# Kernel tuning notes

Hardware: AMD Instinct MI355X
Metric: run time of the kernel (lower is better)

The kernel has to match this reference:

```python
import jax, jax.numpy as jnp
import numpy as np

B, V = 256, 128000


def setup_inputs() -> dict:
    key = jax.random.key(0)
    k1, k2 = jax.random.split(key)
    logits = jax.random.normal(k1, (B, V), dtype=jnp.float32)
    temperatures = jax.random.uniform(k2, (B,), dtype=jnp.float32)
    return {"logits": logits, "temperatures": temperatures}


def reference(logits, temperatures):
    # logits: (B, V) float32, temperatures: (B,) float32
    logits = logits.astype(jnp.float32)
    # greedy path (temperature == 0)
    greedy_tokens = jnp.argmax(logits, axis=-1)
    # temperature-scaled softmax; guard t==0 (torch divides by 0 -> nan probs,
    # but the final where() discards that lane, so safe-div is math-equivalent)
    t = temperatures[:, None]
    safe_t = jnp.where(t == 0.0, 1.0, t)
    probs = jax.nn.softmax(logits / safe_t, axis=-1)  # (B, V)
    # Gumbel-max trick as in torch: argmax(probs / Exp(1) noise)
    noise = jax.random.exponential(jax.random.key(1), probs.shape, dtype=jnp.float32)
    sample_tokens = jnp.argmax(probs / noise, axis=-1)
    return jnp.where(temperatures == 0.0, greedy_tokens, sample_tokens)
```

## Files before the change

### kernel.cpp

```cpp
#include <hip/hip_runtime.h>
#include <stdint.h>
#include <math.h>

constexpr int BROWS = 256;
constexpr int VCOLS = 128000;
constexpr int NQ    = 5;
constexpr int QCOLS = VCOLS / NQ;
constexpr int QV4   = QCOLS / 4;
constexpr int NBLK  = BROWS * NQ;
constexpr int NTHR  = 320;
constexpr int NITER = QV4 / (NTHR * 4);

__device__ __forceinline__ uint32_t fmap(float v) {
  uint32_t b = __float_as_uint(v);
  return b ^ (uint32_t)(((int32_t)b >> 31) | 0x80000000);
}

__device__ __forceinline__ unsigned long long mkkey(uint32_t s, int idx) {
  return ((unsigned long long)s << 32) | (uint32_t)(~(uint32_t)idx);
}

__device__ __forceinline__ uint32_t rotl(uint32_t x, uint32_t r) {
  return __builtin_amdgcn_alignbit(x, x, 32u - r);
}

__device__ __forceinline__ void tf4_bits(uint32_t i0, uint32_t i1, uint32_t i2,
                                         uint32_t i3, uint32_t o[4]) {
  uint32_t a0, a1, a2, a3;
  uint32_t b0 = i0, b1 = i1, b2 = i2, b3 = i3;
#define RND(r) \
  a0 += b0; b0 = rotl(b0, r) ^ a0; \
  a1 += b1; b1 = rotl(b1, r) ^ a1; \
  a2 += b2; b2 = rotl(b2, r) ^ a2; \
  a3 += b3; b3 = rotl(b3, r) ^ a3;
  a0 = b0; b0 = rotl(b0, 13u) ^ a0;
  a1 = b1; b1 = rotl(b1, 13u) ^ a1;
  a2 = b2; b2 = rotl(b2, 13u) ^ a2;
  a3 = b3; b3 = rotl(b3, 13u) ^ a3;
  RND(15u) RND(26u) RND(6u)
  a0 += 1u; a1 += 1u; a2 += 1u; a3 += 1u;
  b0 += 0x1BD11BDCu; b1 += 0x1BD11BDCu; b2 += 0x1BD11BDCu; b3 += 0x1BD11BDCu;
  RND(17u) RND(29u) RND(16u) RND(24u)
  a0 += 0x1BD11BDBu; a1 += 0x1BD11BDBu; a2 += 0x1BD11BDBu; a3 += 0x1BD11BDBu;
  b0 += 2u; b1 += 2u; b2 += 2u; b3 += 2u;
  RND(13u) RND(15u) RND(26u) RND(6u)
  b0 += 4u; b1 += 4u; b2 += 4u; b3 += 4u;
  RND(17u) RND(29u) RND(16u) RND(24u)
  a0 += 1u; a1 += 1u; a2 += 1u; a3 += 1u;
  b0 += 0x1BD11BDFu; b1 += 0x1BD11BDFu; b2 += 0x1BD11BDFu; b3 += 0x1BD11BDFu;
  RND(13u) RND(15u) RND(26u) RND(6u)
  a0 += 0x1BD11BDBu; a1 += 0x1BD11BDBu; a2 += 0x1BD11BDBu; a3 += 0x1BD11BDBu;
  b0 += 5u; b1 += 5u; b2 += 5u; b3 += 5u;
#undef RND
  o[0] = a0 ^ b0; o[1] = a1 ^ b1; o[2] = a2 ^ b2; o[3] = a3 ^ b3;
}

template <int NT>
__device__ __forceinline__ unsigned long long blockMaxU64(unsigned long long v) {
  __shared__ unsigned long long s_w[NT / 64];
  const int wid = threadIdx.x >> 6, lane = threadIdx.x & 63;
  #pragma unroll
  for (int off = 32; off > 0; off >>= 1) {
    unsigned long long o = __shfl_xor(v, off, 64);
    if (o > v) v = o;
  }
  if (lane == 0) s_w[wid] = v;
  __syncthreads();
  if (threadIdx.x == 0) {
    #pragma unroll
    for (int w = 1; w < NT / 64; ++w) if (s_w[w] > v) v = s_w[w];
    s_w[0] = v;
  }
  __syncthreads();
  return s_w[0];
}

extern "C" __global__ void __launch_bounds__(NTHR)
k_main(const float* __restrict__ logits,
       const float* __restrict__ temps,
       unsigned long long* __restrict__ gPart,
       unsigned long long* __restrict__ sPart)
{
  const int blk = blockIdx.x;
  const int row = blk / NQ, q = blk % NQ;
  const float4* base =
      reinterpret_cast<const float4*>(logits + (size_t)row * VCOLS + q * QCOLS);

  const float t = temps[row];
  const float safe_t = (t == 0.0f) ? 1.0f : t;
  const float c1 = (1.0f / safe_t) * 1.4426950408889634f;

  const uint32_t rowbase = (uint32_t)row * (uint32_t)VCOLS;
  const uint32_t Ce = rowbase + (uint32_t)(q * QCOLS) + 1u;

  float gv = -INFINITY; uint32_t gx = 0u;
  float bv = -INFINITY; uint32_t bx = 0u;

  int vb = (int)threadIdx.x;
  float4 A0 = base[vb], A1 = base[vb + NTHR],
         A2 = base[vb + 2 * NTHR], A3 = base[vb + 3 * NTHR];

  #pragma unroll 1
  for (int it = 0; it < NITER; ++it) {
    const int nvb = vb + 4 * NTHR;
    float4 B0, B1, B2, B3;
    if (it + 1 < NITER) {
      B0 = base[nvb]; B1 = base[nvb + NTHR];
      B2 = base[nvb + 2 * NTHR]; B3 = base[nvb + 3 * NTHR];
    }

    const float4 As[4] = {A0, A1, A2, A3};
    #pragma unroll
    for (int u = 0; u < 4; ++u) {
      const uint32_t ce = Ce + (uint32_t)((vb + u * NTHR) * 4);
      const float lx[4] = {As[u].x, As[u].y, As[u].z, As[u].w};
      uint32_t bits[4];
      tf4_bits(ce, ce + 1u, ce + 2u, ce + 3u, bits);
      #pragma unroll
      for (uint32_t k = 0; k < 4; ++k) {
        const uint32_t x1i = ce + k;
        float f = __uint_as_float((bits[k] >> 9) | 0x3F800000u);
        float g = __builtin_amdgcn_logf(2.0f - f);
        float g2 = __builtin_amdgcn_logf(fabsf(g));
        float val = fmaf(lx[k], c1, -g2);
        if (lx[k] > gv) { gv = lx[k]; gx = x1i; }
        if (val  > bv) { bv = val;    bx = x1i; }
      }
    }

    vb = nvb;
    A0 = B0; A1 = B1; A2 = B2; A3 = B3;
  }

  const int gcol = (int)(gx - 1u - rowbase);
  const int scol = (int)(bx - 1u - rowbase);
  unsigned long long gk = blockMaxU64<NTHR>(mkkey(fmap(gv), gcol));
  unsigned long long sk = blockMaxU64<NTHR>(mkkey(fmap(bv), scol));
  if (threadIdx.x == 0) { gPart[blk] = gk; sPart[blk] = sk; }
}

extern "C" __global__ void __launch_bounds__(BROWS)
k3_final(const float* __restrict__ temps,
         const unsigned long long* __restrict__ gPart,
         const unsigned long long* __restrict__ sPart,
         int* __restrict__ out)
{
  const int r = threadIdx.x;
  if (r >= BROWS) return;
  unsigned long long g = gPart[r * NQ];
  unsigned long long s = sPart[r * NQ];
  #pragma unroll
  for (int j = 1; j < NQ; ++j) {
    unsigned long long og = gPart[r * NQ + j];
    unsigned long long os = sPart[r * NQ + j];
    if (og > g) g = og;
    if (os > s) s = os;
  }
  const int greedy = (int)(~(uint32_t)g);
  const int samp   = (int)(~(uint32_t)s);
  out[r] = (temps[r] == 0.0f) ? greedy : samp;
}

extern "C" void kernel_launch(void* const* d_in, const int* in_sizes, int n_in,
                              void* d_out, int out_size, void* d_ws, size_t ws_size,
                              hipStream_t stream) {
  const float* logits = (const float*)d_in[0];
  const float* temps  = (const float*)d_in[1];
  int* out = (int*)d_out;

  unsigned long long* gPart = (unsigned long long*)d_ws;
  unsigned long long* sPart = gPart + NBLK;

  k_main<<<NBLK, NTHR, 0, stream>>>(logits, temps, gPart, sPart);
  k3_final<<<1, BROWS, 0, stream>>>(temps, gPart, sPart, out);
}
```

Before: 81.72 us.

## Split greedy argmax into separate kernel run only for zero-temperature rows

Takes the greedy argmax tracking out of the main sampling loop. A new kernel computes the greedy max only for rows whose temperature is zero and returns early for all other rows. The row split doubles from 5 to 10 chunks, with a 2-deep float4 prefetch in place of 4-deep, to give more blocks. The cost is an extra kernel launch and a second read of the logits for any greedy rows. The random test temperatures are almost never exactly zero, so in practice that kernel mostly exits.

```diff
diff --git a/kernel.cpp b/kernel.cpp
--- a/kernel.cpp
+++ b/kernel.cpp
@@ -4,12 +4,12 @@
 
 constexpr int BROWS = 256;
 constexpr int VCOLS = 128000;
-constexpr int NQ    = 5;
+constexpr int NQ    = 10;
 constexpr int QCOLS = VCOLS / NQ;
 constexpr int QV4   = QCOLS / 4;
 constexpr int NBLK  = BROWS * NQ;
 constexpr int NTHR  = 320;
-constexpr int NITER = QV4 / (NTHR * 4);
+constexpr int NITER = QV4 / (NTHR * 2);
 
 __device__ __forceinline__ uint32_t fmap(float v) {
   uint32_t b = __float_as_uint(v);
@@ -78,7 +78,6 @@
 extern "C" __global__ void __launch_bounds__(NTHR)
 k_main(const float* __restrict__ logits,
        const float* __restrict__ temps,
-       unsigned long long* __restrict__ gPart,
        unsigned long long* __restrict__ sPart)
 {
   const int blk = blockIdx.x;
@@ -93,50 +92,73 @@
   const uint32_t rowbase = (uint32_t)row * (uint32_t)VCOLS;
   const uint32_t Ce = rowbase + (uint32_t)(q * QCOLS) + 1u;
 
-  float gv = -INFINITY; uint32_t gx = 0u;
   float bv = -INFINITY; uint32_t bx = 0u;
 
   int vb = (int)threadIdx.x;
-  float4 A0 = base[vb], A1 = base[vb + NTHR],
-         A2 = base[vb + 2 * NTHR], A3 = base[vb + 3 * NTHR];
+  float4 A0 = base[vb], A1 = base[vb + NTHR];
 
   #pragma unroll 1
   for (int it = 0; it < NITER; ++it) {
-    const int nvb = vb + 4 * NTHR;
-    float4 B0, B1, B2, B3;
+    const int nvb = vb + 2 * NTHR;
+    float4 B0, B1;
     if (it + 1 < NITER) {
       B0 = base[nvb]; B1 = base[nvb + NTHR];
-      B2 = base[nvb + 2 * NTHR]; B3 = base[nvb + 3 * NTHR];
     }
 
-    const float4 As[4] = {A0, A1, A2, A3};
+    const float4 As[2] = {A0, A1};
     #pragma unroll
-    for (int u = 0; u < 4; ++u) {
+    for (int u = 0; u < 2; ++u) {
       const uint32_t ce = Ce + (uint32_t)((vb + u * NTHR) * 4);
       const float lx[4] = {As[u].x, As[u].y, As[u].z, As[u].w};
       uint32_t bits[4];
       tf4_bits(ce, ce + 1u, ce + 2u, ce + 3u, bits);
       #pragma unroll
       for (uint32_t k = 0; k < 4; ++k) {
-        const uint32_t x1i = ce + k;
         float f = __uint_as_float((bits[k] >> 9) | 0x3F800000u);
         float g = __builtin_amdgcn_logf(2.0f - f);
         float g2 = __builtin_amdgcn_logf(fabsf(g));
         float val = fmaf(lx[k], c1, -g2);
-        if (lx[k] > gv) { gv = lx[k]; gx = x1i; }
-        if (val  > bv) { bv = val;    bx = x1i; }
+        if (val > bv) { bv = val; bx = ce + k; }
       }
     }
 
     vb = nvb;
-    A0 = B0; A1 = B1; A2 = B2; A3 = B3;
+    A0 = B0; A1 = B1;
   }
 
-  const int gcol = (int)(gx - 1u - rowbase);
   const int scol = (int)(bx - 1u - rowbase);
-  unsigned long long gk = blockMaxU64<NTHR>(mkkey(fmap(gv), gcol));
   unsigned long long sk = blockMaxU64<NTHR>(mkkey(fmap(bv), scol));
-  if (threadIdx.x == 0) { gPart[blk] = gk; sPart[blk] = sk; }
+  if (threadIdx.x == 0) sPart[blk] = sk;
+}
+
+extern "C" __global__ void __launch_bounds__(NTHR)
+k1_greedy(const float* __restrict__ logits,
+          const float* __restrict__ temps,
+          unsigned long long* __restrict__ gPart)
+{
+  const int blk = blockIdx.x;
+  const int row = blk / NQ, q = blk % NQ;
+  if (temps[row] != 0.0f) return;
+
+  const float4* base =
+      reinterpret_cast<const float4*>(logits + (size_t)row * VCOLS + q * QCOLS);
+  const int idx0 = q * QCOLS;
+
+  unsigned long long best = 0ull;
+  for (int vv = threadIdx.x; vv < QV4; vv += NTHR) {
+    float4 l4 = base[vv];
+    int v0 = idx0 + vv * 4;
+    unsigned long long k0 = mkkey(fmap(l4.x), v0 + 0);
+    unsigned long long k1 = mkkey(fmap(l4.y), v0 + 1);
+    unsigned long long k2 = mkkey(fmap(l4.z), v0 + 2);
+    unsigned long long k3 = mkkey(fmap(l4.w), v0 + 3);
+    if (k1 > k0) k0 = k1;
+    if (k3 > k2) k2 = k3;
+    if (k2 > k0) k0 = k2;
+    if (k0 > best) best = k0;
+  }
+  best = blockMaxU64<NTHR>(best);
+  if (threadIdx.x == 0) gPart[blk] = best;
 }
 
 extern "C" __global__ void __launch_bounds__(BROWS)
@@ -147,18 +169,18 @@
 {
   const int r = threadIdx.x;
   if (r >= BROWS) return;
-  unsigned long long g = gPart[r * NQ];
-  unsigned long long s = sPart[r * NQ];
+  const bool greedy_row = (temps[r] == 0.0f);
+  unsigned long long g = 0ull, s = 0ull;
   #pragma unroll
-  for (int j = 1; j < NQ; ++j) {
-    unsigned long long og = gPart[r * NQ + j];
+  for (int j = 0; j < NQ; ++j) {
+    if (greedy_row) {
+      unsigned long long og = gPart[r * NQ + j];
+      if (og > g) g = og;
+    }
     unsigned long long os = sPart[r * NQ + j];
-    if (og > g) g = og;
     if (os > s) s = os;
   }
-  const int greedy = (int)(~(uint32_t)g);
-  const int samp   = (int)(~(uint32_t)s);
-  out[r] = (temps[r] == 0.0f) ? greedy : samp;
+  out[r] = greedy_row ? (int)(~(uint32_t)g) : (int)(~(uint32_t)s);
 }
 
 extern "C" void kernel_launch(void* const* d_in, const int* in_sizes, int n_in,
@@ -171,6 +193,7 @@
   unsigned long long* gPart = (unsigned long long*)d_ws;
   unsigned long long* sPart = gPart + NBLK;
 
-  k_main<<<NBLK, NTHR, 0, stream>>>(logits, temps, gPart, sPart);
+  k_main<<<NBLK, NTHR, 0, stream>>>(logits, temps, sPart);
+  k1_greedy<<<NBLK, NTHR, 0, stream>>>(logits, temps, gPart);
   k3_final<<<1, BROWS, 0, stream>>>(temps, gPart, sPart, out);
 }
```

Result: slower. 100.2 us (+22.7%).
